# Kernel optimization log

Measured on AMD Instinct MI355X. Metric: run time of the kernel, lower is better.

The kernel has to match this reference:

```python
import jax, jax.numpy as jnp
import numpy as np

B, N, E, H, R, L, VOCAB, KINDS = 8, 4096, 524288, 128, 8, 2, 100000, 8


def setup_inputs() -> dict:
    key = jax.random.key(0)
    ks = jax.random.split(key, 12)
    concept_ids = jax.random.randint(ks[0], (B, N), 1, VOCAB)  # avoid padding_idx 0
    kind_ids = jax.random.randint(ks[1], (B, N), 0, KINDS)
    node_mask = jnp.ones((B, N), dtype=jnp.int32)
    # edges constrained within each batch block (module assumes per-subgraph edges)
    e_batch = jax.random.randint(ks[2], (E,), 0, B)
    src = e_batch * N + jax.random.randint(ks[3], (E,), 0, N)
    dst = e_batch * N + jax.random.randint(ks[4], (E,), 0, N)
    edge_index = jnp.stack([src, dst], axis=0)
    edge_type = jax.random.randint(ks[5], (E,), 0, R)
    s = 0.02
    concept_emb = jax.random.normal(ks[6], (VOCAB, H), jnp.float32) * s
    concept_emb = concept_emb.at[0].set(0.0)  # padding_idx=0
    kind_emb = jax.random.normal(ks[7], (KINDS, H), jnp.float32) * s
    proj_W = jax.random.normal(ks[8], (H, H), jnp.float32) * s
    proj_b = jnp.zeros((H,), jnp.float32)
    self_W = jax.random.normal(ks[9], (L, H, H), jnp.float32) * s
    self_b = jnp.zeros((L, H), jnp.float32)
    rel_W = jax.random.normal(ks[10], (L, R, H, H), jnp.float32) * s
    return dict(pkg_node_concept_ids=concept_ids, pkg_node_kind_ids=kind_ids,
                pkg_node_mask=node_mask, pkg_edge_index=edge_index,
                pkg_edge_type=edge_type, concept_emb=concept_emb, kind_emb=kind_emb,
                proj_W=proj_W, proj_b=proj_b, self_W=self_W, self_b=self_b, rel_W=rel_W)


def reference(pkg_node_concept_ids, pkg_node_kind_ids, pkg_node_mask,
              pkg_edge_index, pkg_edge_type, concept_emb, kind_emb,
              proj_W, proj_b, self_W, self_b, rel_W):
    b, n = pkg_node_concept_ids.shape
    num_nodes = b * n
    # input embedding + projection (dropout = identity in eval)
    x = concept_emb[pkg_node_concept_ids] + kind_emb[pkg_node_kind_ids]  # [B,N,H]
    x = jnp.einsum('bnh,gh->bng', x, proj_W) + proj_b
    x = x.reshape(num_nodes, -1)  # packed node states [B*N, H]
    src, dst = pkg_edge_index[0], pkg_edge_index[1]
    deg = jax.ops.segment_sum(jnp.ones_like(src, dtype=x.dtype), dst,
                              num_segments=num_nodes)[:, None]
    deg = jnp.maximum(deg, 1.0)
    n_layers, n_rel = rel_W.shape[0], rel_W.shape[1]
    for l in range(n_layers):
        xs = x[src]  # [E,H] gather
        msgs = jnp.zeros_like(xs)
        for r in range(n_rel):
            msgs = msgs + jnp.where((pkg_edge_type == r)[:, None],
                                    xs @ rel_W[l, r].T, 0.0)
        agg = jax.ops.segment_sum(msgs, dst, num_segments=num_nodes) / deg
        x = jax.nn.relu(x @ self_W[l].T + self_b[l] + agg)
    out = x.reshape(b, n, -1) * pkg_node_mask[..., None].astype(x.dtype)
    return out
```

## Files before the change

### kernel.cpp

```cpp
#include <hip/hip_runtime.h>
#include <hip/hip_bf16.h>

#define NODES 32768
#define HD 128
#define NE 524288
#define NR 8
#define NS 262144
#define PASSB 65536

typedef unsigned int u32;
typedef unsigned short u16;
typedef __attribute__((ext_vector_type(8))) short bf16x8;
typedef __attribute__((ext_vector_type(4))) float f32x4;

#define XH_OFF   (0u)
#define XL_OFF   (8u<<20)
#define XH2_OFF  (16u<<20)
#define XL2_OFF  (24u<<20)
#define ADJ_OFF  (32u<<20)
#define RP_OFF   (34u<<20)
#define CUR_OFF  (36u<<20)
#define BSUM_OFF (37u<<20)
#define BP_OFF   (38u<<20)

#define BP_LAYER 294912
#define PP_ELEM  589824

__device__ __forceinline__ float bflo(u32 u){ union{u32 i;float f;}c; c.i=u<<16; return c.f; }
__device__ __forceinline__ float bfhi(u32 u){ union{u32 i;float f;}c; c.i=u&0xffff0000u; return c.f; }
__device__ __forceinline__ u16 f2bf(float f){
  u32 u=__float_as_uint(f);
  u32 r=u + 0x7fffu + ((u>>16)&1u);
  return (u16)(r>>16);
}
__device__ __forceinline__ float bf2f(u16 h){ return __uint_as_float(((u32)h)<<16); }

__device__ __forceinline__ void gl_lds16(const void* g, void* l){
  __builtin_amdgcn_global_load_lds((const __attribute__((address_space(1))) u32*)g,
                                   (__attribute__((address_space(3))) u32*)l, 16, 0, 0);
}

__global__ void prep_w(const float* __restrict__ rW, const float* __restrict__ sW,
                       const float* __restrict__ pWg, u16* __restrict__ Bp)
{
  int idx=blockIdx.x*256+threadIdx.x;
  if(idx<294912){
    int l=idx/147456;
    int rem=idx%147456;
    int t=rem>>14;
    int kn=rem&16383;
    int k=kn>>7, n=kn&127;
    float w;
    if(t<8) w=rW[(((size_t)l*NR+t)*HD+n)*HD+k];
    else    w=sW[((size_t)l*HD+n)*HD+k];
    u16* base=Bp+(size_t)l*BP_LAYER+(size_t)t*32768;
    int ks=k>>5, q=(k>>3)&3, j=k&7;
    size_t off=((size_t)ks*128+n)*32+q*8+j;
    u16 hb=f2bf(w);
    u16 lb=f2bf(w-bf2f(hb));
    base[off]=hb;
    base[off+16384]=lb;
  } else {
    int kn=idx-294912;
    int k=kn>>7, n=kn&127;
    float w=pWg[(size_t)n*HD+k];
    u16* base=Bp+PP_ELEM;
    int ks=k>>5, q=(k>>3)&3, j=k&7;
    size_t off=((size_t)ks*128+n)*32+q*8+j;
    u16 hb=f2bf(w);
    u16 lb=f2bf(w-bf2f(hb));
    base[off]=hb;
    base[off+16384]=lb;
  }
}

__global__ __launch_bounds__(256,2) void embed_mfma(
    const int* __restrict__ cid, const int* __restrict__ kid,
    const float* __restrict__ cemb, const float* __restrict__ kemb,
    const u16* __restrict__ PP, const float* __restrict__ pb,
    u16* __restrict__ xh, u16* __restrict__ xl)
{
  __shared__ u16 Atile[2][128*128];
  const int tid=threadIdx.x;
  const int wave=tid>>6, lane=tid&63;
  const int wm=wave>>1, wn=wave&1;
  const int q=lane>>4;
  const int d0=blockIdx.x*128;

  { int r=tid>>1, half=tid&1;
    int ci=cid[d0+r], ki=kid[d0+r];
    const float* cp=cemb+(size_t)ci*HD+half*64;
    const float* kp=kemb+(size_t)ki*HD+half*64;
#pragma unroll
    for(int cc=0;cc<8;cc++){
      float4 a0=*(const float4*)(cp+cc*8);
      float4 a1=*(const float4*)(cp+cc*8+4);
      float4 b0=*(const float4*)(kp+cc*8);
      float4 b1=*(const float4*)(kp+cc*8+4);
      float v[8]={a0.x+b0.x,a0.y+b0.y,a0.z+b0.z,a0.w+b0.w,
                  a1.x+b1.x,a1.y+b1.y,a1.z+b1.z,a1.w+b1.w};
      u16 hb[8], lb[8];
#pragma unroll
      for(int j=0;j<8;j++){ hb[j]=f2bf(v[j]); lb[j]=f2bf(v[j]-bf2f(hb[j])); }
      int chunk=half*8+cc;
      int dst=r*128+(chunk^(r&15))*8;
      uint4 hv={(u32)hb[0]|((u32)hb[1]<<16),(u32)hb[2]|((u32)hb[3]<<16),
                (u32)hb[4]|((u32)hb[5]<<16),(u32)hb[6]|((u32)hb[7]<<16)};
      uint4 lv={(u32)lb[0]|((u32)lb[1]<<16),(u32)lb[2]|((u32)lb[3]<<16),
                (u32)lb[4]|((u32)lb[5]<<16),(u32)lb[6]|((u32)lb[7]<<16)};
      *(uint4*)&Atile[0][dst]=hv;
      *(uint4*)&Atile[1][dst]=lv;
    }
  }
  __syncthreads();

  f32x4 acc[4][4];
#pragma unroll
  for(int a=0;a<4;a++)
#pragma unroll
    for(int b=0;b<4;b++) acc[a][b]=(f32x4){0.f,0.f,0.f,0.f};

#pragma unroll
  for(int ks=0;ks<4;ks++){
    bf16x8 ah[4];
#pragma unroll
    for(int tm=0;tm<4;tm++){
      int m=wm*64+tm*16+(lane&15);
      ah[tm]=*(const bf16x8*)&Atile[0][m*128+(((ks*4)+q)^(m&15))*8];
    }
#pragma unroll
    for(int s=0;s<2;s++){
      const u16* Bb=PP+s*16384;
#pragma unroll
      for(int tn=0;tn<4;tn++){
        int n=wn*64+tn*16+(lane&15);
        bf16x8 bfr=*(const bf16x8*)&Bb[((size_t)ks*128+n)*32+q*8];
#pragma unroll
        for(int tm=0;tm<4;tm++)
          acc[tm][tn]=__builtin_amdgcn_mfma_f32_16x16x32_bf16(ah[tm],bfr,acc[tm][tn],0,0,0);
      }
    }
  }
#pragma unroll
  for(int ks=0;ks<4;ks++){
    bf16x8 al[4];
#pragma unroll
    for(int tm=0;tm<4;tm++){
      int m=wm*64+tm*16+(lane&15);
      al[tm]=*(const bf16x8*)&Atile[1][m*128+(((ks*4)+q)^(m&15))*8];
    }
#pragma unroll
    for(int tn=0;tn<4;tn++){
      int n=wn*64+tn*16+(lane&15);
      bf16x8 bfr=*(const bf16x8*)&PP[((size_t)ks*128+n)*32+q*8];
#pragma unroll
      for(int tm=0;tm<4;tm++)
        acc[tm][tn]=__builtin_amdgcn_mfma_f32_16x16x32_bf16(al[tm],bfr,acc[tm][tn],0,0,0);
    }
  }

#pragma unroll
  for(int tn=0;tn<4;tn++){
    int n=wn*64+tn*16+(lane&15);
    float b=pb[n];
#pragma unroll
    for(int tm=0;tm<4;tm++){
      int rbase=d0+wm*64+tm*16+q*4;
#pragma unroll
      for(int r=0;r<4;r++){
        float v=acc[tm][tn][r]+b;
        u16 hb=f2bf(v);
        u16 lb=f2bf(v-bf2f(hb));
        xh[(size_t)(rbase+r)*HD+n]=hb;
        xl[(size_t)(rbase+r)*HD+n]=lb;
      }
    }
  }
}

__global__ void count_deg2(const int* __restrict__ dst, const int* __restrict__ et,
                           u32* __restrict__ cnt){
  int e=blockIdx.x*256+threadIdx.x;
  int t=et[e];
  int key=(t>>1)*PASSB + dst[e]*2 + (t&1);
  atomicAdd(&cnt[key],1u);
}

__global__ void scan1(u32* __restrict__ cnt, u32* __restrict__ rp, u32* __restrict__ bsum){
  __shared__ u32 sh[256];
  int t=threadIdx.x; int base=blockIdx.x*256;
  u32 v=cnt[base+t]; sh[t]=v;
  cnt[base+t]=0u;
  __syncthreads();
  for(int off=1;off<256;off<<=1){
    u32 tv=(t>=off)?sh[t-off]:0u; __syncthreads();
    sh[t]+=tv; __syncthreads();
  }
  rp[base+t]=sh[t]-v;
  if(t==255) bsum[blockIdx.x]=sh[255];
}

__global__ void scan2b(u32* __restrict__ bsum, u32* __restrict__ rp){
  __shared__ u32 sh[256];
  int t=threadIdx.x;
  u32 v0=bsum[t*4+0],v1=bsum[t*4+1],v2=bsum[t*4+2],v3=bsum[t*4+3];
  u32 s=v0+v1+v2+v3;
  sh[t]=s; __syncthreads();
  for(int off=1;off<256;off<<=1){
    u32 tv=(t>=off)?sh[t-off]:0u; __syncthreads();
    sh[t]+=tv; __syncthreads();
  }
  u32 ex=sh[t]-s;
  bsum[t*4+0]=ex; bsum[t*4+1]=ex+v0; bsum[t*4+2]=ex+v0+v1; bsum[t*4+3]=ex+v0+v1+v2;
  if(t==0) rp[NS]=NE;
  if(t==255) bsum[1024]=0u;
}

__global__ void scatter_edges2(const int* __restrict__ src, const int* __restrict__ dst,
                               const int* __restrict__ et, const u32* __restrict__ rp,
                               const u32* __restrict__ bsum,
                               u32* __restrict__ cur, u32* __restrict__ adj){
  int e=blockIdx.x*256+threadIdx.x;
  int t=et[e];
  int d=dst[e];
  int key=(t>>1)*PASSB + d*2 + (t&1);
  u32 pos=atomicAdd(&cur[key],1u);
  u32 val=(u32)src[e] | (((u32)(((t&1)<<5)|(d&31)))<<15);
  adj[rp[key]+bsum[key>>8]+pos]=val;
}

#define FLUSHROW(rw,a0,a1) do{ \
  u16 fh0=f2bf(a0), fh1=f2bf(a1); \
  u16 fl0=f2bf((a0)-bf2f(fh0)), fl1=f2bf((a1)-bf2f(fh1)); \
  int fw=(rw)*64 + (((lane>>2)^((rw)&15))<<2) + (lane&3); \
  ((u32*)As[0])[fw]=(u32)fh0|((u32)fh1<<16); \
  ((u32*)As[1])[fw]=(u32)fl0|((u32)fl1<<16); \
}while(0)

__global__ __launch_bounds__(256,4) void fused_layer(
    const u16* __restrict__ xh, const u16* __restrict__ xl,
    const u16* __restrict__ Bp,
    const u32* __restrict__ rp, const u32* __restrict__ bsum,
    const u32* __restrict__ adj,
    const float* __restrict__ sb, const int* __restrict__ mask,
    u16* __restrict__ oh, u16* __restrict__ ol, float* __restrict__ outf, int last)
{
  __shared__ u16 As[2][64*128];
  __shared__ float sdeg[32];
  const int tid=threadIdx.x;
  const int wave=tid>>6, lane=tid&63;
  const int q=lane>>4;
  const int d0=blockIdx.x*32;
  const u32* xh32=(const u32*)xh;
  const u32* xl32=(const u32*)xl;

  f32x4 accR[2][2], accS[2][2];
#pragma unroll
  for(int a=0;a<2;a++)
#pragma unroll
    for(int b=0;b<2;b++){ accR[a][b]=(f32x4){0.f,0.f,0.f,0.f}; accS[a][b]=(f32x4){0.f,0.f,0.f,0.f}; }

  for(int p=0;p<4;p++){
    { uint4 zz={0u,0u,0u,0u};
#pragma unroll
      for(int rl=0;rl<2;rl++)
#pragma unroll
        for(int i=0;i<2;i++){
          int row=rl*32+wave*8+i*4+(lane>>4);
          int col16=lane&15;
          *(uint4*)&As[0][row*128+col16*8]=zz;
          *(uint4*)&As[1][row*128+col16*8]=zz;
        }
    }
    { u32 k0=(u32)(p*PASSB + (d0+wave*8)*2);
      u32 begW=rp[k0]+bsum[k0>>8];
      u32 k1=k0+16;
      u32 endW=rp[k1]+bsum[k1>>8];
      int currow=-1; float v0=0.f,v1=0.f;
      for(u32 base=begW; base<endW; base+=64){
        int nk=(int)(endW-base); if(nk>64) nk=64;
        u32 adjv=(lane<nk)?adj[base+lane]:0u;
        int i=0;
        for(; i+4<=nk; i+=4){
          u32 w0=(u32)__shfl((int)adjv,i+0);
          u32 w1=(u32)__shfl((int)adjv,i+1);
          u32 w2=(u32)__shfl((int)adjv,i+2);
          u32 w3=(u32)__shfl((int)adjv,i+3);
          u32 h0=xh32[(size_t)(w0&0x7fffu)*64+lane], l0=xl32[(size_t)(w0&0x7fffu)*64+lane];
          u32 h1=xh32[(size_t)(w1&0x7fffu)*64+lane], l1=xl32[(size_t)(w1&0x7fffu)*64+lane];
          u32 h2=xh32[(size_t)(w2&0x7fffu)*64+lane], l2=xl32[(size_t)(w2&0x7fffu)*64+lane];
          u32 h3=xh32[(size_t)(w3&0x7fffu)*64+lane], l3=xl32[(size_t)(w3&0x7fffu)*64+lane];
          int r0=(int)(w0>>15);
          if(r0!=currow){ if(currow>=0) FLUSHROW(currow,v0,v1); currow=r0; v0=0.f; v1=0.f; }
          v0+=bflo(h0)+bflo(l0); v1+=bfhi(h0)+bfhi(l0);
          int r1=(int)(w1>>15);
          if(r1!=currow){ FLUSHROW(currow,v0,v1); currow=r1; v0=0.f; v1=0.f; }
          v0+=bflo(h1)+bflo(l1); v1+=bfhi(h1)+bfhi(l1);
          int r2=(int)(w2>>15);
          if(r2!=currow){ FLUSHROW(currow,v0,v1); currow=r2; v0=0.f; v1=0.f; }
          v0+=bflo(h2)+bflo(l2); v1+=bfhi(h2)+bfhi(l2);
          int r3=(int)(w3>>15);
          if(r3!=currow){ FLUSHROW(currow,v0,v1); currow=r3; v0=0.f; v1=0.f; }
          v0+=bflo(h3)+bflo(l3); v1+=bfhi(h3)+bfhi(l3);
        }
        for(; i<nk; i++){
          u32 w0=(u32)__shfl((int)adjv,i);
          u32 h=xh32[(size_t)(w0&0x7fffu)*64+lane], l=xl32[(size_t)(w0&0x7fffu)*64+lane];
          int r0=(int)(w0>>15);
          if(r0!=currow){ if(currow>=0) FLUSHROW(currow,v0,v1); currow=r0; v0=0.f; v1=0.f; }
          v0+=bflo(h)+bflo(l); v1+=bfhi(h)+bfhi(l);
        }
      }
      if(currow>=0) FLUSHROW(currow,v0,v1);
    }
    __syncthreads();
#pragma unroll
    for(int rl=0;rl<2;rl++){
      const u16* Bt=Bp+(size_t)(p*2+rl)*32768;
#pragma unroll
      for(int ks=0;ks<4;ks++){
        bf16x8 ah[2],al[2];
#pragma unroll
        for(int mf=0;mf<2;mf++){
          int ar=rl*32+mf*16+(lane&15);
          int off=ar*128+((((ks<<2)+q)^(ar&15))<<3);
          ah[mf]=*(const bf16x8*)&As[0][off];
          al[mf]=*(const bf16x8*)&As[1][off];
        }
#pragma unroll
        for(int tn=0;tn<2;tn++){
          int n=wave*32+tn*16+(lane&15);
          size_t boff=((size_t)(ks*128+n))*32+q*8;
          bf16x8 bh=*(const bf16x8*)&Bt[boff];
          bf16x8 bl=*(const bf16x8*)&Bt[boff+16384];
#pragma unroll
          for(int mf=0;mf<2;mf++){
            accR[mf][tn]=__builtin_amdgcn_mfma_f32_16x16x32_bf16(ah[mf],bh,accR[mf][tn],0,0,0);
            accR[mf][tn]=__builtin_amdgcn_mfma_f32_16x16x32_bf16(al[mf],bh,accR[mf][tn],0,0,0);
            accR[mf][tn]=__builtin_amdgcn_mfma_f32_16x16x32_bf16(ah[mf],bl,accR[mf][tn],0,0,0);
          }
        }
      }
    }
    __syncthreads();
  }

#pragma unroll
  for(int i=0;i<2;i++){
    int rbase=wave*8+i*4;
    int r=rbase+(lane>>4);
    int g=(lane&15)^(r&15);
    gl_lds16(xh+(size_t)(d0+r)*HD+g*8, &As[0][rbase*128]);
  }
#pragma unroll
  for(int i=0;i<2;i++){
    int rbase=wave*8+i*4;
    int r=rbase+(lane>>4);
    int g=(lane&15)^(r&15);
    gl_lds16(xl+(size_t)(d0+r)*HD+g*8, &As[1][rbase*128]);
  }
  if(tid<32){
    int g=d0+tid; u32 dg=0;
#pragma unroll
    for(int ph=0;ph<4;ph++){
      u32 k=(u32)(ph*PASSB+g*2);
      dg+=(rp[k+2]+bsum[(k+2)>>8])-(rp[k]+bsum[k>>8]);
    }
    sdeg[tid]=1.f/fmaxf((float)dg,1.f);
  }
  __syncthreads();
  { const u16* Bt=Bp+(size_t)8*32768;
#pragma unroll
    for(int ks=0;ks<4;ks++){
      bf16x8 ah[2],al[2];
#pragma unroll
      for(int mf=0;mf<2;mf++){
        int ar=mf*16+(lane&15);
        int off=ar*128+((((ks<<2)+q)^(ar&15))<<3);
        ah[mf]=*(const bf16x8*)&As[0][off];
        al[mf]=*(const bf16x8*)&As[1][off];
      }
#pragma unroll
      for(int tn=0;tn<2;tn++){
        int n=wave*32+tn*16+(lane&15);
        size_t boff=((size_t)(ks*128+n))*32+q*8;
        bf16x8 bh=*(const bf16x8*)&Bt[boff];
        bf16x8 bl=*(const bf16x8*)&Bt[boff+16384];
#pragma unroll
        for(int mf=0;mf<2;mf++){
          accS[mf][tn]=__builtin_amdgcn_mfma_f32_16x16x32_bf16(ah[mf],bh,accS[mf][tn],0,0,0);
          accS[mf][tn]=__builtin_amdgcn_mfma_f32_16x16x32_bf16(al[mf],bh,accS[mf][tn],0,0,0);
          accS[mf][tn]=__builtin_amdgcn_mfma_f32_16x16x32_bf16(ah[mf],bl,accS[mf][tn],0,0,0);
        }
      }
    }
  }

#pragma unroll
  for(int tn=0;tn<2;tn++){
    int n=wave*32+tn*16+(lane&15);
    float bb=sb[n];
    if(last){
#pragma unroll
      for(int mf=0;mf<2;mf++)
#pragma unroll
        for(int rr=0;rr<4;rr++){
          int row=mf*16+q*4+rr;
          float v=fmaxf(accS[mf][tn][rr]+bb+accR[mf][tn][rr]*sdeg[row],0.f);
          v*=(float)mask[d0+row];
          outf[(size_t)(d0+row)*HD+n]=v;
        }
    } else {
#pragma unroll
      for(int mf=0;mf<2;mf++)
#pragma unroll
        for(int rr=0;rr<4;rr++){
          int row=mf*16+q*4+rr;
          float v=fmaxf(accS[mf][tn][rr]+bb+accR[mf][tn][rr]*sdeg[row],0.f);
          u16 hb=f2bf(v);
          u16 lb=f2bf(v-bf2f(hb));
          oh[(size_t)(d0+row)*HD+n]=hb;
          ol[(size_t)(d0+row)*HD+n]=lb;
        }
    }
  }
}

extern "C" void kernel_launch(void* const* d_in, const int* in_sizes, int n_in,
                              void* d_out, int out_size, void* d_ws, size_t ws_size,
                              hipStream_t stream)
{
  (void)in_sizes; (void)n_in; (void)out_size; (void)ws_size;
  const int*   cid =(const int*)  d_in[0];
  const int*   kid =(const int*)  d_in[1];
  const int*   mask=(const int*)  d_in[2];
  const int*   ei  =(const int*)  d_in[3];
  const int*   et  =(const int*)  d_in[4];
  const float* cemb=(const float*)d_in[5];
  const float* kemb=(const float*)d_in[6];
  const float* pW  =(const float*)d_in[7];
  const float* pb  =(const float*)d_in[8];
  const float* sW  =(const float*)d_in[9];
  const float* sb  =(const float*)d_in[10];
  const float* rW  =(const float*)d_in[11];
  float* out=(float*)d_out;
  char*  ws =(char*)d_ws;

  u16* xh =(u16*)(ws+XH_OFF);
  u16* xl =(u16*)(ws+XL_OFF);
  u16* xh2=(u16*)(ws+XH2_OFF);
  u16* xl2=(u16*)(ws+XL2_OFF);
  u32* adj =(u32*)(ws+ADJ_OFF);
  u32* rp  =(u32*)(ws+RP_OFF);
  u32* cur =(u32*)(ws+CUR_OFF);
  u32* bsum=(u32*)(ws+BSUM_OFF);
  u16* Bp  =(u16*)(ws+BP_OFF);
  const int* srcA=ei;
  const int* dstA=ei+NE;

  hipMemsetAsync(cur,0,NS*sizeof(u32),stream);
  prep_w<<<1216,256,0,stream>>>(rW,sW,pW,Bp);
  embed_mfma<<<NODES/128,256,0,stream>>>(cid,kid,cemb,kemb,Bp+PP_ELEM,pb,xh,xl);
  count_deg2<<<NE/256,256,0,stream>>>(dstA,et,cur);
  scan1<<<NS/256,256,0,stream>>>(cur,rp,bsum);
  scan2b<<<1,256,0,stream>>>(bsum,rp);
  scatter_edges2<<<NE/256,256,0,stream>>>(srcA,dstA,et,rp,bsum,cur,adj);

  fused_layer<<<NODES/32,256,0,stream>>>(xh,xl,Bp,rp,bsum,adj,sb,mask,xh2,xl2,out,0);
  fused_layer<<<NODES/32,256,0,stream>>>(xh2,xl2,Bp+BP_LAYER,rp,bsum,adj,sb+HD,mask,xh,xl,out,1);
}
```

Measured before the change: 317.2 us.

## Gather only bf16-high node states, batch 8 loads, stage projection output via LDS

The edge aggregation loop now gathers only the high bf16 half of each source node state and drops the low-residual load. It uses readlane instead of shuffle and issues 8 independent loads before accumulating. The flush uses bit masking instead of conversion calls, and the projection epilogue goes through swizzled LDS so global stores are 16-byte coalesced. Dropping the residual halves the gather traffic but lowers the precision of the neighbour sums to plain bf16, which risks tolerance failures.

```diff
diff --git a/kernel.cpp b/kernel.cpp
--- a/kernel.cpp
+++ b/kernel.cpp
@@ -159,21 +159,42 @@
     }
   }
 
-#pragma unroll
-  for(int tn=0;tn<4;tn++){
-    int n=wn*64+tn*16+(lane&15);
-    float b=pb[n];
-#pragma unroll
-    for(int tm=0;tm<4;tm++){
-      int rbase=d0+wm*64+tm*16+q*4;
-#pragma unroll
-      for(int r=0;r<4;r++){
-        float v=acc[tm][tn][r]+b;
-        u16 hb=f2bf(v);
-        u16 lb=f2bf(v-bf2f(hb));
-        xh[(size_t)(rbase+r)*HD+n]=hb;
-        xl[(size_t)(rbase+r)*HD+n]=lb;
-      }
+  __syncthreads();
+  { u16* Sh=(u16*)Atile[0];
+    u16* Sl=(u16*)Atile[1];
+#pragma unroll
+    for(int tn=0;tn<4;tn++){
+      int n=wn*64+tn*16+(lane&15);
+      float b=pb[n];
+#pragma unroll
+      for(int tm=0;tm<4;tm++){
+        int rbase=wm*64+tm*16+q*4;
+#pragma unroll
+        for(int r=0;r<4;r++){
+          float v=acc[tm][tn][r]+b;
+          u16 hb=f2bf(v);
+          u16 lb=f2bf(v-bf2f(hb));
+          int row=rbase+r;
+          u32 ab=(u32)(row*256+n*2);
+          ab^=((u32)((row>>2)&3))<<5;
+          Sh[ab>>1]=hb;
+          Sl[ab>>1]=lb;
+        }
+      }
+    }
+  }
+  __syncthreads();
+  { const char* S0=(const char*)Atile[0];
+    const char* S1=(const char*)Atile[1];
+    char* xhb=(char*)(xh+(size_t)d0*HD);
+    char* xlb=(char*)(xl+(size_t)d0*HD);
+#pragma unroll
+    for(int i=0;i<8;i++){
+      u32 byte=(u32)(i*256+tid)*16;
+      u32 row=byte>>8;
+      u32 lb2=byte^((((row>>2)&3))<<5);
+      *(uint4*)(xhb+byte)=*(const uint4*)(S0+lb2);
+      *(uint4*)(xlb+byte)=*(const uint4*)(S1+lb2);
     }
   }
 }
@@ -229,12 +250,16 @@
   adj[rp[key]+bsum[key>>8]+pos]=val;
 }
 
-#define FLUSHROW(rw,a0,a1) do{ \
-  u16 fh0=f2bf(a0), fh1=f2bf(a1); \
-  u16 fl0=f2bf((a0)-bf2f(fh0)), fl1=f2bf((a1)-bf2f(fh1)); \
+#define FLUSH2(rw) do{ \
+  u32 u0=__float_as_uint(v0), u1=__float_as_uint(v1); \
+  u32 t0=u0&0xffff0000u, t1=u1&0xffff0000u; \
+  u32 hp=t1|(u0>>16); \
+  float l0f=v0-__uint_as_float(t0), l1f=v1-__uint_as_float(t1); \
+  u32 w0b=__float_as_uint(l0f), w1b=__float_as_uint(l1f); \
+  u32 lp=(w1b&0xffff0000u)|(w0b>>16); \
   int fw=(rw)*64 + (((lane>>2)^((rw)&15))<<2) + (lane&3); \
-  ((u32*)As[0])[fw]=(u32)fh0|((u32)fh1<<16); \
-  ((u32*)As[1])[fw]=(u32)fl0|((u32)fl1<<16); \
+  ((u32*)As[0])[fw]=hp; \
+  ((u32*)As[1])[fw]=lp; \
 }while(0)
 
 __global__ __launch_bounds__(256,4) void fused_layer(
@@ -252,7 +277,6 @@
   const int q=lane>>4;
   const int d0=blockIdx.x*32;
   const u32* xh32=(const u32*)xh;
-  const u32* xl32=(const u32*)xl;
 
   f32x4 accR[2][2], accS[2][2];
 #pragma unroll
@@ -275,43 +299,37 @@
     { u32 k0=(u32)(p*PASSB + (d0+wave*8)*2);
       u32 begW=rp[k0]+bsum[k0>>8];
       u32 k1=k0+16;
-      u32 endW=rp[k1]+bsum[k1>>8];
+      u32 endW=rp[k1]+bsum[(k1)>>8];
       int currow=-1; float v0=0.f,v1=0.f;
       for(u32 base=begW; base<endW; base+=64){
         int nk=(int)(endW-base); if(nk>64) nk=64;
         u32 adjv=(lane<nk)?adj[base+lane]:0u;
         int i=0;
-        for(; i+4<=nk; i+=4){
-          u32 w0=(u32)__shfl((int)adjv,i+0);
-          u32 w1=(u32)__shfl((int)adjv,i+1);
-          u32 w2=(u32)__shfl((int)adjv,i+2);
-          u32 w3=(u32)__shfl((int)adjv,i+3);
-          u32 h0=xh32[(size_t)(w0&0x7fffu)*64+lane], l0=xl32[(size_t)(w0&0x7fffu)*64+lane];
-          u32 h1=xh32[(size_t)(w1&0x7fffu)*64+lane], l1=xl32[(size_t)(w1&0x7fffu)*64+lane];
-          u32 h2=xh32[(size_t)(w2&0x7fffu)*64+lane], l2=xl32[(size_t)(w2&0x7fffu)*64+lane];
-          u32 h3=xh32[(size_t)(w3&0x7fffu)*64+lane], l3=xl32[(size_t)(w3&0x7fffu)*64+lane];
-          int r0=(int)(w0>>15);
-          if(r0!=currow){ if(currow>=0) FLUSHROW(currow,v0,v1); currow=r0; v0=0.f; v1=0.f; }
-          v0+=bflo(h0)+bflo(l0); v1+=bfhi(h0)+bfhi(l0);
-          int r1=(int)(w1>>15);
-          if(r1!=currow){ FLUSHROW(currow,v0,v1); currow=r1; v0=0.f; v1=0.f; }
-          v0+=bflo(h1)+bflo(l1); v1+=bfhi(h1)+bfhi(l1);
-          int r2=(int)(w2>>15);
-          if(r2!=currow){ FLUSHROW(currow,v0,v1); currow=r2; v0=0.f; v1=0.f; }
-          v0+=bflo(h2)+bflo(l2); v1+=bfhi(h2)+bfhi(l2);
-          int r3=(int)(w3>>15);
-          if(r3!=currow){ FLUSHROW(currow,v0,v1); currow=r3; v0=0.f; v1=0.f; }
-          v0+=bflo(h3)+bflo(l3); v1+=bfhi(h3)+bfhi(l3);
+        for(; i+8<=nk; i+=8){
+          u32 ww[8]; u32 hv[8];
+#pragma unroll
+          for(int j=0;j<8;j++){
+            ww[j]=(u32)__builtin_amdgcn_readlane((int)adjv,i+j);
+            hv[j]=xh32[(size_t)(ww[j]&0x7fffu)*64+lane];
+          }
+#pragma unroll
+          for(int j=0;j<8;j++){
+            int r=(int)(ww[j]>>15);
+            if(r!=currow){ if(currow>=0) FLUSH2(currow); currow=r; v0=0.f; v1=0.f; }
+            v0+=__uint_as_float(hv[j]<<16);
+            v1+=__uint_as_float(hv[j]&0xffff0000u);
+          }
         }
         for(; i<nk; i++){
-          u32 w0=(u32)__shfl((int)adjv,i);
-          u32 h=xh32[(size_t)(w0&0x7fffu)*64+lane], l=xl32[(size_t)(w0&0x7fffu)*64+lane];
-          int r0=(int)(w0>>15);
-          if(r0!=currow){ if(currow>=0) FLUSHROW(currow,v0,v1); currow=r0; v0=0.f; v1=0.f; }
-          v0+=bflo(h)+bflo(l); v1+=bfhi(h)+bfhi(l);
-        }
-      }
-      if(currow>=0) FLUSHROW(currow,v0,v1);
+          u32 w=(u32)__builtin_amdgcn_readlane((int)adjv,i);
+          u32 h=xh32[(size_t)(w&0x7fffu)*64+lane];
+          int r=(int)(w>>15);
+          if(r!=currow){ if(currow>=0) FLUSH2(currow); currow=r; v0=0.f; v1=0.f; }
+          v0+=__uint_as_float(h<<16);
+          v1+=__uint_as_float(h&0xffff0000u);
+        }
+      }
+      if(currow>=0) FLUSH2(currow);
     }
     __syncthreads();
 #pragma unroll
```

Result: faster. 301.2 us (-5.0%).
